# Performance work log

Measured on AMD Instinct MI355X. Metric: run time of the kernel, lower is better.

The kernel has to match this reference:

```python
import jax, jax.numpy as jnp
import numpy as np

STRIDE = 14
C_LOCAL = 2
NUM_HEADS = 12


def sparse_attention_mask(n_tokens, stride_length=STRIDE, c=C_LOCAL, mode='fixed'):
    q = jnp.arange(n_tokens)[:, None]  # row index Q
    k = jnp.arange(n_tokens)[None, :]  # col index K
    if mode == 'fixed':
        m1 = (q // stride_length) == (k // stride_length)
        m2 = ((k % stride_length) >= stride_length - c) & ((k % stride_length) <= stride_length)
        return m1 | m2
    elif mode == 'strided':
        m1 = jnp.abs(q - k) <= stride_length
        m2 = ((q - k) % stride_length) == 0
        return m1 | m2


def setup_inputs() -> dict:
    key = jax.random.key(0)
    ks = jax.random.split(key, 5)
    B, N, C = 16, 1024, 768
    return {
        'x': jax.random.normal(ks[0], (B, N, C), dtype=jnp.float32),
        'w_qkv': jax.random.normal(ks[1], (3 * C, C), dtype=jnp.float32) * (1.0 / np.sqrt(C)),
        'b_qkv': jax.random.normal(ks[2], (3 * C,), dtype=jnp.float32) * 0.02,
        'w_proj': jax.random.normal(ks[3], (C, C), dtype=jnp.float32) * (1.0 / np.sqrt(C)),
        'b_proj': jax.random.normal(ks[4], (C,), dtype=jnp.float32) * 0.02,
    }


def reference(x, w_qkv, b_qkv, w_proj, b_proj):
    B, N, C = x.shape
    H = NUM_HEADS
    D = C // H
    mask = sparse_attention_mask(N, mode='fixed')  # [N, N] bool

    # qkv projection: [B,N,3C] -> [3,B,H,N,D]
    qkv = x @ w_qkv.T + b_qkv
    qkv = qkv.reshape(B, N, 3, H, D).transpose(2, 0, 3, 1, 4)
    q, k, v = qkv[0], qkv[1], qkv[2]

    # SDPA with default scale = 1/sqrt(head_dim) and boolean attn_mask
    scale = 1.0 / jnp.sqrt(jnp.asarray(D, dtype=x.dtype))
    scores = jnp.einsum('bhnd,bhmd->bhnm', q, k) * scale
    scores = jnp.where(mask[None, None, :, :], scores, jnp.finfo(scores.dtype).min)
    attn = jax.nn.softmax(scores, axis=-1)
    out = jnp.einsum('bhnm,bhmd->bhnd', attn, v)

    # merge heads and output projection
    out = out.transpose(0, 2, 1, 3).reshape(B, N, C)
    return out @ w_proj.T + b_proj
```

## Files before the change

kernel.cpp:

```cpp
#include <hip/hip_runtime.h>
#include <stdint.h>

typedef unsigned short u16;
typedef __attribute__((ext_vector_type(8))) short bf16x8;
typedef __attribute__((ext_vector_type(4))) short s16x4;
typedef __attribute__((ext_vector_type(4))) float f32x4;

__device__ __forceinline__ u16 f2bf(float f) {
  uint32_t x = __builtin_bit_cast(uint32_t, f);
  uint32_t r = (x + 0x7fffu + ((x >> 16) & 1u)) >> 16;
  return (u16)r;
}
__device__ __forceinline__ float bf2f(u16 u) {
  return __builtin_bit_cast(float, (uint32_t)u << 16);
}

typedef __attribute__((address_space(3))) uint32_t lds_u32;
typedef const __attribute__((address_space(1))) uint32_t glb_u32;
__device__ __forceinline__ void gload_lds16(const void* g, void* l) {
  __builtin_amdgcn_global_load_lds(
      reinterpret_cast<glb_u32*>(reinterpret_cast<uintptr_t>(g)),
      reinterpret_cast<lds_u32*>(reinterpret_cast<uintptr_t>(l)),
      16, 0, 0);
}

__device__ __forceinline__ int swz(int r) { return (r & 3) ^ ((r >> 2) & 3); }

__global__ void cvt_split_kernel(const float* __restrict__ in, u16* __restrict__ hi,
                                 u16* __restrict__ lo, int n4) {
  typedef __attribute__((ext_vector_type(4))) float float4v;
  int i = blockIdx.x * 256 + threadIdx.x;
  const int stride = gridDim.x * 256;
  for (; i < n4; i += stride) {
    float4v v = *(const float4v*)(in + (size_t)i * 4);
    s16x4 hv;
#pragma unroll
    for (int j = 0; j < 4; ++j) hv[j] = (short)f2bf(v[j]);
    *(s16x4*)(hi + (size_t)i * 4) = hv;
    if (lo) {
      s16x4 lv;
#pragma unroll
      for (int j = 0; j < 4; ++j) lv[j] = (short)f2bf(v[j] - bf2f((u16)hv[j]));
      *(s16x4*)(lo + (size_t)i * 4) = lv;
    }
  }
}

template <int OUTF32>
__global__ __launch_bounds__(256, 3) void gemm_bt(
    const u16* __restrict__ A, const u16* __restrict__ B0,
    const float* __restrict__ bias, float* __restrict__ outF, u16* __restrict__ outB,
    int Ndim, int Kdim) {
  __shared__ u16 sA[3][128 * 32];
  __shared__ u16 sB[3][128 * 32];

  const int tid = threadIdx.x;
  const int lane = tid & 63;
  const int wid = tid >> 6;
  const int wr = wid >> 1;
  const int wc = wid & 1;
  const int brow = blockIdx.x * 128;
  const int bcol = blockIdx.y * 128;
  const int colL = lane & 15;
  const int kgrp = lane >> 4;
  const int NT = Kdim >> 5;

  int srcA[2], srcB[2], ldsU[2];
#pragma unroll
  for (int j = 0; j < 2; ++j) {
    const int u = j * 256 + tid;
    const int r = u >> 2;
    const int sl = (u & 3) ^ swz(r);
    srcA[j] = (brow + r) * Kdim + sl * 8;
    srcB[j] = (bcol + r) * Kdim + sl * 8;
    ldsU[j] = u * 8;
  }

  int oa[4], ob[4];
#pragma unroll
  for (int m = 0; m < 4; ++m) {
    const int r = wr * 64 + m * 16 + colL;
    oa[m] = r * 32 + ((kgrp ^ swz(r)) * 8);
  }
#pragma unroll
  for (int n = 0; n < 4; ++n) {
    const int r = wc * 64 + n * 16 + colL;
    ob[n] = r * 32 + ((kgrp ^ swz(r)) * 8);
  }

  auto stage = [&](int buf, int t) {
    const int k0 = t << 5;
#pragma unroll
    for (int j = 0; j < 2; ++j) {
      gload_lds16(A + (size_t)(srcA[j] + k0), &sA[buf][ldsU[j]]);
      gload_lds16(B0 + (size_t)(srcB[j] + k0), &sB[buf][ldsU[j]]);
    }
  };

  f32x4 acc[4][4] = {};

  stage(0, 0);
  stage(1, 1);
  asm volatile("s_waitcnt vmcnt(4)" ::: "memory");
  __builtin_amdgcn_s_barrier();

  for (int t = 0; t < NT; ++t) {
    const int cur = t % 3;
    if (t + 2 < NT) stage((t + 2) % 3, t + 2);

    bf16x8 a[4], b[4];
#pragma unroll
    for (int m = 0; m < 4; ++m) a[m] = *(const bf16x8*)&sA[cur][oa[m]];
#pragma unroll
    for (int n = 0; n < 4; ++n) b[n] = *(const bf16x8*)&sB[cur][ob[n]];

    __builtin_amdgcn_s_setprio(1);
#pragma unroll
    for (int m = 0; m < 4; ++m)
#pragma unroll
      for (int n = 0; n < 4; ++n)
        acc[m][n] = __builtin_amdgcn_mfma_f32_16x16x32_bf16(a[m], b[n], acc[m][n], 0, 0, 0);
    __builtin_amdgcn_s_setprio(0);

    if (t + 2 < NT)
      asm volatile("s_waitcnt vmcnt(4)" ::: "memory");
    else if (t + 1 < NT)
      asm volatile("s_waitcnt vmcnt(0)" ::: "memory");
    __builtin_amdgcn_s_barrier();
  }

  const int r0 = kgrp * 4;
#pragma unroll
  for (int n = 0; n < 4; ++n) {
    const int colg = bcol + wc * 64 + n * 16 + colL;
    const float bv = bias[colg];
#pragma unroll
    for (int m = 0; m < 4; ++m) {
      const int rowg = brow + wr * 64 + m * 16 + r0;
#pragma unroll
      for (int r = 0; r < 4; ++r) {
        const float v = acc[m][n][r] + bv;
        if (OUTF32)
          outF[(size_t)(rowg + r) * Ndim + colg] = v;
        else
          outB[(size_t)(rowg + r) * Ndim + colg] = f2bf(v);
      }
    }
  }
}

__global__ __launch_bounds__(256) void transpose_v_kernel(const u16* __restrict__ qkv,
                                                          u16* __restrict__ vt) {
  __shared__ u16 t[64][72];
  const int tid = threadIdx.x;
  const int nt = blockIdx.x, h = blockIdx.y, b = blockIdx.z;
  const u16* src = qkv + (size_t)(b * 1024 + nt * 64) * 2304 + 1536 + h * 64;
#pragma unroll
  for (int j = 0; j < 2; ++j) {
    const int c = j * 256 + tid;
    const int row = c >> 3;
    const int off = (c & 7) * 8;
    *(bf16x8*)&t[row][off] = *(const bf16x8*)(src + (size_t)row * 2304 + off);
  }
  __syncthreads();
  u16* dst = vt + (size_t)(b * 12 + h) * 64 * 1024 + nt * 64;
#pragma unroll
  for (int j = 0; j < 2; ++j) {
    const int c = j * 256 + tid;
    const int drow = c >> 3;
    const int noff = (c & 7) * 8;
    bf16x8 o;
#pragma unroll
    for (int i = 0; i < 8; ++i) o[i] = (short)t[noff + i][drow];
    *(bf16x8*)(dst + (size_t)drow * 1024 + noff) = o;
  }
}

__global__ __launch_bounds__(256) void gather_global_kernel(const u16* __restrict__ qkv,
                                                            u16* __restrict__ kgc,
                                                            u16* __restrict__ vgc) {
  __shared__ u16 tl[192][72];
  const int tid = threadIdx.x;
  const int h = blockIdx.x % 12;
  const int b = blockIdx.x / 12;
  const u16* Kg = qkv + (size_t)(b * 1024) * 2304 + 768 + h * 64;
  const u16* Vg = qkv + (size_t)(b * 1024) * 2304 + 1536 + h * 64;
  u16* kout = kgc + (size_t)blockIdx.x * 192 * 64;
  u16* vout = vgc + (size_t)blockIdx.x * 64 * 192;

  for (int t = tid; t < 1536; t += 256) {
    const int s = t >> 3, ch = t & 7;
    bf16x8 kv = {}, vv = {};
    if (s < 146) {
      const int tok = (s >> 1) * 14 + 12 + (s & 1);
      kv = *(const bf16x8*)(Kg + (size_t)tok * 2304 + ch * 8);
      vv = *(const bf16x8*)(Vg + (size_t)tok * 2304 + ch * 8);
    }
    *(bf16x8*)(kout + s * 64 + ch * 8) = kv;
    *(bf16x8*)&tl[s][ch * 8] = vv;
  }
  __syncthreads();
  for (int t = tid; t < 64 * 24; t += 256) {
    const int d = t / 24, c8 = (t % 24) * 8;
    bf16x8 o;
#pragma unroll
    for (int i = 0; i < 8; ++i) o[i] = (short)tl[c8 + i][d];
    *(bf16x8*)(vout + (size_t)d * 192 + c8) = o;
  }
}

__global__ __launch_bounds__(256, 2) void attn_kernel(const u16* __restrict__ qkv,
                                                      const u16* __restrict__ vt,
                                                      const u16* __restrict__ kgc,
                                                      const u16* __restrict__ vgc,
                                                      u16* __restrict__ ao) {
  __shared__ u16 sQ[64 * 64];
  __shared__ u16 sK[2][64 * 64];
  __shared__ u16 sV[2][64 * 64];
  __shared__ u16 sP[4][16 * 72];

  const int tid = threadIdx.x;
  const int lane = tid & 63;
  const int wid = tid >> 6;
  const int qt = blockIdx.x, h = blockIdx.y, b = blockIdx.z;
  const int q0 = qt * 64;
  const int colL = lane & 15;
  const int kgrp = lane >> 4;
  const int bh = b * 12 + h;

  const u16* Qg = qkv + (size_t)(b * 1024 + q0) * 2304 + h * 64;
  const u16* Kg = qkv + (size_t)(b * 1024) * 2304 + 768 + h * 64;
  const u16* Vt = vt + (size_t)bh * 64 * 1024;
  const u16* Kc = kgc + (size_t)bh * 192 * 64;
  const u16* Vc = vgc + (size_t)bh * 64 * 192;

  const int first_blk = q0 / 14;
  const int tok0a = (first_blk * 14) & ~7;

  auto stage_kv = [&](int buf, int it) {
    if (it < 3) {
#pragma unroll
      for (int j = 0; j < 2; ++j) {
        const int c = j * 256 + tid;
        const int row = c >> 3;
        const int sb = ((c & 7) * 16) ^ ((row & 7) << 4);
        gload_lds16((const char*)(Kc + (size_t)(it * 64 + row) * 64) + sb, &sK[buf][c * 8]);
        gload_lds16((const char*)(Vc + (size_t)row * 192 + it * 64) + sb, &sV[buf][c * 8]);
      }
    } else {
      const int tc0 = tok0a + (it - 3) * 64;
#pragma unroll
      for (int j = 0; j < 2; ++j) {
        const int c = j * 256 + tid;
        const int row = c >> 3;
        const int sb = ((c & 7) * 16) ^ ((row & 7) << 4);
        const int ktok = min(tc0 + row, 1023);
        gload_lds16((const char*)(Kg + (size_t)ktok * 2304) + sb, &sK[buf][c * 8]);
        const int vb = min(tc0 * 2 + sb, 2032);
        gload_lds16((const char*)(Vt + (size_t)row * 1024) + vb, &sV[buf][c * 8]);
      }
    }
  };

#pragma unroll
  for (int j = 0; j < 2; ++j) {
    const int c = j * 256 + tid;
    const int row = c >> 3;
    const int off = (c & 7) * 8;
    gload_lds16(Qg + (size_t)row * 2304 + off, &sQ[c * 8]);
  }
  stage_kv(0, 0);
  __syncthreads();

  bf16x8 qf[2];
#pragma unroll
  for (int ks = 0; ks < 2; ++ks)
    qf[ks] = *(const bf16x8*)&sQ[(wid * 16 + colL) * 64 + ks * 32 + kgrp * 8];

  int qblk[4];
#pragma unroll
  for (int r = 0; r < 4; ++r) qblk[r] = (q0 + wid * 16 + kgrp * 4 + r) / 14;

  const float SCL = 0.125f * 1.44269504088896f;
  const float NEG = -3e38f;
  float mrun[4] = {NEG, NEG, NEG, NEG};
  float lsum[4] = {0.f, 0.f, 0.f, 0.f};
  f32x4 oacc[4] = {};

  for (int it = 0; it < 5; ++it) {
    const int cur = it & 1;
    if (it + 1 < 5) stage_kv(cur ^ 1, it + 1);

    f32x4 s[4] = {};
#pragma unroll
    for (int n = 0; n < 4; ++n) {
      const int row = n * 16 + colL;
#pragma unroll
      for (int ks = 0; ks < 2; ++ks) {
        const int cb = (ks * 32 + kgrp * 8) * 2;
        bf16x8 kf = *(const bf16x8*)((const char*)&sK[cur][0] + row * 128 + (cb ^ ((row & 7) << 4)));
        s[n] = __builtin_amdgcn_mfma_f32_16x16x32_bf16(qf[ks], kf, s[n], 0, 0, 0);
      }
    }

    float sv[4][4];
    if (it < 3) {
#pragma unroll
      for (int n = 0; n < 4; ++n) {
        const bool gv = (it * 64 + n * 16 + colL) < 146;
#pragma unroll
        for (int r = 0; r < 4; ++r) sv[n][r] = gv ? s[n][r] * SCL : NEG;
      }
    } else {
      const int tc0 = tok0a + (it - 3) * 64;
#pragma unroll
      for (int n = 0; n < 4; ++n) {
        const int t = tc0 + n * 16 + colL;
        const int tb = t / 14;
        const bool cv = (t < 1024) && ((t - tb * 14) < 12);
#pragma unroll
        for (int r = 0; r < 4; ++r) {
          const bool ok = cv && (tb == qblk[r]);
          sv[n][r] = ok ? s[n][r] * SCL : NEG;
        }
      }
    }

    float pmax[4];
#pragma unroll
    for (int r = 0; r < 4; ++r) {
      float v = fmaxf(fmaxf(sv[0][r], sv[1][r]), fmaxf(sv[2][r], sv[3][r]));
#pragma unroll
      for (int msk = 1; msk <= 8; msk <<= 1) v = fmaxf(v, __shfl_xor(v, msk));
      pmax[r] = v;
    }

    float corr[4], psum[4];
#pragma unroll
    for (int r = 0; r < 4; ++r) {
      const float mn = fmaxf(mrun[r], pmax[r]);
      corr[r] = exp2f(mrun[r] - mn);
      mrun[r] = mn;
      psum[r] = 0.f;
    }

    float p[4][4];
#pragma unroll
    for (int n = 0; n < 4; ++n)
#pragma unroll
      for (int r = 0; r < 4; ++r) {
        p[n][r] = exp2f(sv[n][r] - mrun[r]);
        psum[r] += p[n][r];
      }

#pragma unroll
    for (int r = 0; r < 4; ++r) {
      float v = psum[r];
#pragma unroll
      for (int msk = 1; msk <= 8; msk <<= 1) v += __shfl_xor(v, msk);
      lsum[r] = lsum[r] * corr[r] + v;
    }

#pragma unroll
    for (int n = 0; n < 4; ++n)
#pragma unroll
      for (int r = 0; r < 4; ++r)
        sP[wid][(kgrp * 4 + r) * 72 + n * 16 + colL] = f2bf(p[n][r]);

#pragma unroll
    for (int dn = 0; dn < 4; ++dn)
#pragma unroll
      for (int r = 0; r < 4; ++r) oacc[dn][r] *= corr[r];

#pragma unroll
    for (int ks = 0; ks < 2; ++ks) {
      bf16x8 pf = *(const bf16x8*)&sP[wid][colL * 72 + ks * 32 + kgrp * 8];
#pragma unroll
      for (int dn = 0; dn < 4; ++dn) {
        const int vrow = dn * 16 + colL;
        const int cb = (ks * 32 + kgrp * 8) * 2;
        bf16x8 vf = *(const bf16x8*)((const char*)&sV[cur][0] + vrow * 128 + (cb ^ ((vrow & 7) << 4)));
        oacc[dn] = __builtin_amdgcn_mfma_f32_16x16x32_bf16(pf, vf, oacc[dn], 0, 0, 0);
      }
    }

    __syncthreads();
  }

  float inv[4];
#pragma unroll
  for (int r = 0; r < 4; ++r) inv[r] = 1.0f / lsum[r];
#pragma unroll
  for (int dn = 0; dn < 4; ++dn)
#pragma unroll
    for (int r = 0; r < 4; ++r) {
      const int rowg = b * 1024 + q0 + wid * 16 + kgrp * 4 + r;
      const int colg = h * 64 + dn * 16 + colL;
      ao[(size_t)rowg * 768 + colg] = f2bf(oacc[dn][r] * inv[r]);
    }
}

extern "C" void kernel_launch(void* const* d_in, const int* in_sizes, int n_in,
                              void* d_out, int out_size, void* d_ws, size_t ws_size,
                              hipStream_t stream) {
  const float* x = (const float*)d_in[0];
  const float* w_qkv = (const float*)d_in[1];
  const float* b_qkv = (const float*)d_in[2];
  const float* w_proj = (const float*)d_in[3];
  const float* b_proj = (const float*)d_in[4];
  float* out = (float*)d_out;

  char* ws = (char*)d_ws;
  size_t off = 0;
  auto alloc = [&](size_t bytes) {
    char* p = ws + off;
    off += (bytes + 255) & ~(size_t)255;
    return p;
  };
  u16* x_bf = (u16*)alloc(16384ull * 768 * 2);
  u16* wq_bf = (u16*)alloc(2304ull * 768 * 2);
  u16* wp_bf = (u16*)alloc(768ull * 768 * 2);
  u16* qkvb = (u16*)alloc(16384ull * 2304 * 2);
  u16* vt = (u16*)alloc(192ull * 64 * 1024 * 2);
  u16* kgc = (u16*)alloc(192ull * 192 * 64 * 2);
  u16* vgc = (u16*)alloc(192ull * 64 * 192 * 2);
  u16* ao = x_bf;

  cvt_split_kernel<<<dim3(4096), dim3(256), 0, stream>>>(x, x_bf, nullptr, 16384 * 768 / 4);
  cvt_split_kernel<<<dim3(1728), dim3(256), 0, stream>>>(w_qkv, wq_bf, nullptr, 2304 * 768 / 4);
  cvt_split_kernel<<<dim3(576), dim3(256), 0, stream>>>(w_proj, wp_bf, nullptr, 768 * 768 / 4);

  gemm_bt<0><<<dim3(128, 18), dim3(256), 0, stream>>>(x_bf, wq_bf, b_qkv,
                                                      nullptr, qkvb, 2304, 768);
  transpose_v_kernel<<<dim3(16, 12, 16), dim3(256), 0, stream>>>(qkvb, vt);
  gather_global_kernel<<<dim3(192), dim3(256), 0, stream>>>(qkvb, kgc, vgc);
  attn_kernel<<<dim3(16, 12, 16), dim3(256), 0, stream>>>(qkvb, vt, kgc, vgc, ao);
  gemm_bt<1><<<dim3(128, 6), dim3(256), 0, stream>>>(ao, wp_bf, b_proj,
                                                     out, nullptr, 768, 768);
}
```

Before: 201.4 us.

## Fuse V transpose into QKV GEMM epilogue and gather V from transposed buffer

Measured after the change: 203.7 us. About the same (+1.2%).

```diff
diff --git a/kernel.cpp b/kernel.cpp
--- a/kernel.cpp
+++ b/kernel.cpp
@@ -46,11 +46,11 @@
   }
 }
 
-template <int OUTF32>
+template <int OUTF32, int VOUT>
 __global__ __launch_bounds__(256, 3) void gemm_bt(
     const u16* __restrict__ A, const u16* __restrict__ B0,
     const float* __restrict__ bias, float* __restrict__ outF, u16* __restrict__ outB,
-    int Ndim, int Kdim) {
+    u16* __restrict__ vtOut, int Ndim, int Kdim) {
   __shared__ u16 sA[3][128 * 32];
   __shared__ u16 sB[3][128 * 32];
 
@@ -137,75 +137,55 @@
 #pragma unroll
     for (int m = 0; m < 4; ++m) {
       const int rowg = brow + wr * 64 + m * 16 + r0;
-#pragma unroll
-      for (int r = 0; r < 4; ++r) {
-        const float v = acc[m][n][r] + bv;
-        if (OUTF32)
-          outF[(size_t)(rowg + r) * Ndim + colg] = v;
-        else
-          outB[(size_t)(rowg + r) * Ndim + colg] = f2bf(v);
-      }
-    }
-  }
-}
-
-__global__ __launch_bounds__(256) void transpose_v_kernel(const u16* __restrict__ qkv,
-                                                          u16* __restrict__ vt) {
-  __shared__ u16 t[64][72];
-  const int tid = threadIdx.x;
-  const int nt = blockIdx.x, h = blockIdx.y, b = blockIdx.z;
-  const u16* src = qkv + (size_t)(b * 1024 + nt * 64) * 2304 + 1536 + h * 64;
-#pragma unroll
-  for (int j = 0; j < 2; ++j) {
-    const int c = j * 256 + tid;
-    const int row = c >> 3;
-    const int off = (c & 7) * 8;
-    *(bf16x8*)&t[row][off] = *(const bf16x8*)(src + (size_t)row * 2304 + off);
-  }
-  __syncthreads();
-  u16* dst = vt + (size_t)(b * 12 + h) * 64 * 1024 + nt * 64;
-#pragma unroll
-  for (int j = 0; j < 2; ++j) {
-    const int c = j * 256 + tid;
-    const int drow = c >> 3;
-    const int noff = (c & 7) * 8;
-    bf16x8 o;
-#pragma unroll
-    for (int i = 0; i < 8; ++i) o[i] = (short)t[noff + i][drow];
-    *(bf16x8*)(dst + (size_t)drow * 1024 + noff) = o;
+      if (VOUT && colg >= 1536) {
+        const int h = (colg - 1536) >> 6;
+        const int d = (colg - 1536) & 63;
+        const int bb = rowg >> 10;
+        const int tok = rowg & 1023;
+        s16x4 pk;
+#pragma unroll
+        for (int r = 0; r < 4; ++r) pk[r] = (short)f2bf(acc[m][n][r] + bv);
+        *(s16x4*)&vtOut[(size_t)(((bb * 12 + h) << 6) + d) * 1024 + tok] = pk;
+      } else {
+#pragma unroll
+        for (int r = 0; r < 4; ++r) {
+          const float v = acc[m][n][r] + bv;
+          if (OUTF32)
+            outF[(size_t)(rowg + r) * Ndim + colg] = v;
+          else
+            outB[(size_t)(rowg + r) * Ndim + colg] = f2bf(v);
+        }
+      }
+    }
   }
 }
 
 __global__ __launch_bounds__(256) void gather_global_kernel(const u16* __restrict__ qkv,
+                                                            const u16* __restrict__ vt,
                                                             u16* __restrict__ kgc,
                                                             u16* __restrict__ vgc) {
-  __shared__ u16 tl[192][72];
   const int tid = threadIdx.x;
   const int h = blockIdx.x % 12;
   const int b = blockIdx.x / 12;
   const u16* Kg = qkv + (size_t)(b * 1024) * 2304 + 768 + h * 64;
-  const u16* Vg = qkv + (size_t)(b * 1024) * 2304 + 1536 + h * 64;
+  const u16* VtS = vt + (size_t)blockIdx.x * 64 * 1024;
   u16* kout = kgc + (size_t)blockIdx.x * 192 * 64;
   u16* vout = vgc + (size_t)blockIdx.x * 64 * 192;
 
   for (int t = tid; t < 1536; t += 256) {
     const int s = t >> 3, ch = t & 7;
-    bf16x8 kv = {}, vv = {};
+    bf16x8 kv = {};
     if (s < 146) {
       const int tok = (s >> 1) * 14 + 12 + (s & 1);
       kv = *(const bf16x8*)(Kg + (size_t)tok * 2304 + ch * 8);
-      vv = *(const bf16x8*)(Vg + (size_t)tok * 2304 + ch * 8);
     }
     *(bf16x8*)(kout + s * 64 + ch * 8) = kv;
-    *(bf16x8*)&tl[s][ch * 8] = vv;
-  }
-  __syncthreads();
-  for (int t = tid; t < 64 * 24; t += 256) {
-    const int d = t / 24, c8 = (t % 24) * 8;
-    bf16x8 o;
-#pragma unroll
-    for (int i = 0; i < 8; ++i) o[i] = (short)tl[c8 + i][d];
-    *(bf16x8*)(vout + (size_t)d * 192 + c8) = o;
+  }
+  for (int t = tid; t < 64 * 192; t += 256) {
+    const int d = t / 192, s = t % 192;
+    u16 v = 0;
+    if (s < 146) v = VtS[(size_t)d * 1024 + (s >> 1) * 14 + 12 + (s & 1)];
+    vout[t] = v;
   }
 }
 
@@ -430,11 +410,10 @@
   cvt_split_kernel<<<dim3(1728), dim3(256), 0, stream>>>(w_qkv, wq_bf, nullptr, 2304 * 768 / 4);
   cvt_split_kernel<<<dim3(576), dim3(256), 0, stream>>>(w_proj, wp_bf, nullptr, 768 * 768 / 4);
 
-  gemm_bt<0><<<dim3(128, 18), dim3(256), 0, stream>>>(x_bf, wq_bf, b_qkv,
-                                                      nullptr, qkvb, 2304, 768);
-  transpose_v_kernel<<<dim3(16, 12, 16), dim3(256), 0, stream>>>(qkvb, vt);
-  gather_global_kernel<<<dim3(192), dim3(256), 0, stream>>>(qkvb, kgc, vgc);
+  gemm_bt<0, 1><<<dim3(128, 18), dim3(256), 0, stream>>>(x_bf, wq_bf, b_qkv,
+                                                         nullptr, qkvb, vt, 2304, 768);
+  gather_global_kernel<<<dim3(192), dim3(256), 0, stream>>>(qkvb, vt, kgc, vgc);
   attn_kernel<<<dim3(16, 12, 16), dim3(256), 0, stream>>>(qkvb, vt, kgc, vgc, ao);
-  gemm_bt<1><<<dim3(128, 6), dim3(256), 0, stream>>>(ao, wp_bf, b_proj,
-                                                     out, nullptr, 768, 768);
-}
+  gemm_bt<1, 0><<<dim3(128, 6), dim3(256), 0, stream>>>(ao, wp_bf, b_proj,
+                                                        out, nullptr, nullptr, 768, 768);
+}
```

## Load GEMM A operand directly from global into registers, double-buffer B in LDS

Applied to the files above, without the earlier changes.

Measured after the change: 270.8 us. 1.34x slower.

```diff
diff --git a/kernel.cpp b/kernel.cpp
--- a/kernel.cpp
+++ b/kernel.cpp
@@ -51,8 +51,7 @@
     const u16* __restrict__ A, const u16* __restrict__ B0,
     const float* __restrict__ bias, float* __restrict__ outF, u16* __restrict__ outB,
     int Ndim, int Kdim) {
-  __shared__ u16 sA[3][128 * 32];
-  __shared__ u16 sB[3][128 * 32];
+  __shared__ u16 sB[2][128 * 32];
 
   const int tid = threadIdx.x;
   const int lane = tid & 63;
@@ -65,52 +64,52 @@
   const int kgrp = lane >> 4;
   const int NT = Kdim >> 5;
 
-  int srcA[2], srcB[2], ldsU[2];
+  int srcB[2], ldsU[2];
 #pragma unroll
   for (int j = 0; j < 2; ++j) {
     const int u = j * 256 + tid;
     const int r = u >> 2;
     const int sl = (u & 3) ^ swz(r);
-    srcA[j] = (brow + r) * Kdim + sl * 8;
     srcB[j] = (bcol + r) * Kdim + sl * 8;
     ldsU[j] = u * 8;
   }
 
-  int oa[4], ob[4];
-#pragma unroll
-  for (int m = 0; m < 4; ++m) {
-    const int r = wr * 64 + m * 16 + colL;
-    oa[m] = r * 32 + ((kgrp ^ swz(r)) * 8);
-  }
+  int ob[4];
 #pragma unroll
   for (int n = 0; n < 4; ++n) {
     const int r = wc * 64 + n * 16 + colL;
     ob[n] = r * 32 + ((kgrp ^ swz(r)) * 8);
   }
 
+  const u16* aP[4];
+#pragma unroll
+  for (int m = 0; m < 4; ++m)
+    aP[m] = A + (size_t)(brow + wr * 64 + m * 16 + colL) * Kdim + kgrp * 8;
+
   auto stage = [&](int buf, int t) {
     const int k0 = t << 5;
 #pragma unroll
-    for (int j = 0; j < 2; ++j) {
-      gload_lds16(A + (size_t)(srcA[j] + k0), &sA[buf][ldsU[j]]);
+    for (int j = 0; j < 2; ++j)
       gload_lds16(B0 + (size_t)(srcB[j] + k0), &sB[buf][ldsU[j]]);
-    }
   };
 
   f32x4 acc[4][4] = {};
+  bf16x8 aC[4], aN[4];
 
   stage(0, 0);
-  stage(1, 1);
-  asm volatile("s_waitcnt vmcnt(4)" ::: "memory");
-  __builtin_amdgcn_s_barrier();
+#pragma unroll
+  for (int m = 0; m < 4; ++m) aC[m] = *(const bf16x8*)aP[m];
+  __syncthreads();
 
   for (int t = 0; t < NT; ++t) {
-    const int cur = t % 3;
-    if (t + 2 < NT) stage((t + 2) % 3, t + 2);
-
-    bf16x8 a[4], b[4];
-#pragma unroll
-    for (int m = 0; m < 4; ++m) a[m] = *(const bf16x8*)&sA[cur][oa[m]];
+    const int cur = t & 1;
+    if (t + 1 < NT) {
+      stage(cur ^ 1, t + 1);
+#pragma unroll
+      for (int m = 0; m < 4; ++m) aN[m] = *(const bf16x8*)(aP[m] + (t + 1) * 32);
+    }
+
+    bf16x8 b[4];
 #pragma unroll
     for (int n = 0; n < 4; ++n) b[n] = *(const bf16x8*)&sB[cur][ob[n]];
 
@@ -119,14 +118,14 @@
     for (int m = 0; m < 4; ++m)
 #pragma unroll
       for (int n = 0; n < 4; ++n)
-        acc[m][n] = __builtin_amdgcn_mfma_f32_16x16x32_bf16(a[m], b[n], acc[m][n], 0, 0, 0);
+        acc[m][n] = __builtin_amdgcn_mfma_f32_16x16x32_bf16(aC[m], b[n], acc[m][n], 0, 0, 0);
     __builtin_amdgcn_s_setprio(0);
 
-    if (t + 2 < NT)
-      asm volatile("s_waitcnt vmcnt(4)" ::: "memory");
-    else if (t + 1 < NT)
-      asm volatile("s_waitcnt vmcnt(0)" ::: "memory");
-    __builtin_amdgcn_s_barrier();
+    if (t + 1 < NT) {
+#pragma unroll
+      for (int m = 0; m < 4; ++m) aC[m] = aN[m];
+    }
+    __syncthreads();
   }
 
   const int r0 = kgrp * 4;
```
